# Kernel optimization log

Measured on AMD Instinct MI355X. Metric: run time of the kernel, lower is better.

## Reference

```python
import jax, jax.numpy as jnp
import numpy as np

K = 3
CHUNK = 1000  # query chunk size for KNN distance tiles
EPS = 1e-8
GRID = 256.0  # coordinate extent (coords / stride in the original)


def _knn3(queries, refs):
    """Brute-force KNN (K=3, squared L2) computed in chunks to bound memory.
    queries: [Q,3], refs: [M,3] -> (dist [Q,3], idx [Q,3] int32)."""
    ref_sq = jnp.sum(refs * refs, axis=-1)  # [M]

    def chunk_fn(q):  # q: [CHUNK,3]
        d = jnp.sum(q * q, -1)[:, None] - 2.0 * (q @ refs.T) + ref_sq[None, :]
        d = jnp.maximum(d, 0.0)  # guard tiny negatives from cancellation
        neg_d, idx = jax.lax.top_k(-d, K)
        return -neg_d, idx

    Q = queries.shape[0]
    qs = queries.reshape(Q // CHUNK, CHUNK, 3)
    dists, idxs = jax.lax.map(chunk_fn, qs)
    return dists.reshape(Q, K), idxs.reshape(Q, K)


def setup_inputs() -> dict:
    key = jax.random.key(0)
    k1, k2, k3, k4 = jax.random.split(key, 4)
    N1, N2, C = 20000, 20000, 8
    xyz1 = jax.random.uniform(k1, (N1, 3), dtype=jnp.float32) * GRID
    point1 = jax.random.normal(k2, (N1, C), dtype=jnp.float32)
    xyz2 = jax.random.uniform(k3, (N2, 3), dtype=jnp.float32) * GRID
    motion = jax.random.normal(k4, (N2, C, 3), dtype=jnp.float32)
    return {"xyz1": xyz1, "point1": point1, "xyz2": xyz2, "motion": motion}


def reference(xyz1, point1, xyz2, motion):
    # Motion-compensated inter prediction tail of inter_prediction.forward:
    # per-channel warp, KNN(K=3) into frame 1, inverse-distance interpolation.
    N2, C, _ = motion.shape
    # xyz2_ = xyz2.unsqueeze(2) + motion -> [N2*C, 3]
    xyz2_ = (xyz2[:, None, :] + motion).reshape(N2 * C, 3)
    dist, idx = _knn3(xyz2_, xyz1)                 # [N2*C,3]
    dist = dist + EPS
    dist = dist.reshape(N2, C, K)
    idx = idx.reshape(N2, C, K)
    weights = 1.0 / dist
    weights = weights / jnp.maximum(weights.sum(axis=2, keepdims=True), 3.0)
    # knn_point1[n,c,k] = point1[idx[n,c,k], c]  (per-channel gather)
    pt = point1.T                                   # [C, N1]
    knn_point1 = pt[jnp.arange(C)[None, :, None], idx]  # [N2,C,3]
    predicted_point2 = (weights * knn_point1).sum(axis=2)  # [N2,C]
    return predicted_point2
```

## Files before the change

kernel.cpp:

```cpp
#include <hip/hip_runtime.h>
#include <math.h>

#define KNN_EPS 1e-8f
#define GH 16.0f
#define GC 16
#define NCELLS (GC * GC * GC)
#define MARGIN 1.0f
#define CAP 384
#define CAPR 64
#define CAPQ 192


__device__ __forceinline__ int cell_coord(float v) {
    int c = (int)floorf(v * (1.0f / GH));
    return min(max(c, 0), GC - 1);
}

__global__ void fused_scatter_kernel(
    const float* __restrict__ xyz1, int n1,
    const float* __restrict__ xyz2,
    const float* __restrict__ motion, int n2, int C,
    int* __restrict__ counts, int* __restrict__ qcounts,
    float4* __restrict__ rbuck, float4* __restrict__ qbuck,
    float4* __restrict__ refspill, int* __restrict__ rsn,
    float4* __restrict__ qspill, int* __restrict__ qsn)
{
#pragma clang fp contract(off)
    int i = blockIdx.x * blockDim.x + threadIdx.x;
    if (i < n1) {
        float x = xyz1[3 * i + 0];
        float y = xyz1[3 * i + 1];
        float z = xyz1[3 * i + 2];
        int cid = (cell_coord(z) * GC + cell_coord(y)) * GC + cell_coord(x);
        int pos = atomicAdd(&counts[cid], 1);
        float4 v = make_float4(x, y, z, __int_as_float(i));
        if (pos < CAPR) rbuck[cid * CAPR + pos] = v;
        else { int sp = atomicAdd(rsn, 1); refspill[sp] = v; }
    }
    int nq = n2 * C;
    if (i < nq) {
        int n = i / C;
        float qx = xyz2[3 * n + 0] + motion[3 * i + 0];
        float qy = xyz2[3 * n + 1] + motion[3 * i + 1];
        float qz = xyz2[3 * n + 2] + motion[3 * i + 2];
        int cid = (cell_coord(qz) * GC + cell_coord(qy)) * GC + cell_coord(qx);
        int pos = atomicAdd(&qcounts[cid], 1);
        float4 v = make_float4(qx, qy, qz, __int_as_float(i));
        if (pos < CAPQ) qbuck[cid * CAPQ + pos] = v;
        else { int sp = atomicAdd(qsn, 1); qspill[sp] = v; }
    }
}

__device__ __forceinline__ void top3_insert_lex(float d, int j,
                                                float& bd0, float& bd1, float& bd2,
                                                int& bi0, int& bi1, int& bi2) {
    if (d < bd2 || (d == bd2 && j < bi2)) {
        if (d < bd1 || (d == bd1 && j < bi1)) {
            bd2 = bd1; bi2 = bi1;
            if (d < bd0 || (d == bd0 && j < bi0)) {
                bd1 = bd0; bi1 = bi0;
                bd0 = d;   bi0 = j;
            } else {
                bd1 = d;   bi1 = j;
            }
        } else {
            bd2 = d;       bi2 = j;
        }
    }
}

__device__ __forceinline__ void eval_candidate(
    float4 r, float qx, float qy, float qz, float qsq,
    float& bd0, float& bd1, float& bd2, int& bi0, int& bi1, int& bi2) {
    int ridx = __float_as_int(r.w);
    float rsq = r.x * r.x + r.y * r.y;
    rsq = rsq + r.z * r.z;
    float t = fmaf(qz, r.z, fmaf(qy, r.y, qx * r.x));
    float h = qsq + rsq;
    float d = fmaxf(fmaf(-2.0f, t, h), 0.0f);
    top3_insert_lex(d, ridx, bd0, bd1, bd2, bi0, bi1, bi2);
}

__device__ __forceinline__ float cert_radius(float qx, float qy, float qz,
                                             int icx, int icy, int icz, int rho) {
    float R = INFINITY;
    if (icx - rho > 0)      R = fminf(R, qx - (float)(icx - rho) * GH);
    if (icx + rho < GC - 1) R = fminf(R, (float)(icx + rho + 1) * GH - qx);
    if (icy - rho > 0)      R = fminf(R, qy - (float)(icy - rho) * GH);
    if (icy + rho < GC - 1) R = fminf(R, (float)(icy + rho + 1) * GH - qy);
    if (icz - rho > 0)      R = fminf(R, qz - (float)(icz - rho) * GH);
    if (icz + rho < GC - 1) R = fminf(R, (float)(icz + rho + 1) * GH - qz);
    return R;
}

__device__ __forceinline__ void epilogue_store(
    float bd0, float bd1, float bd2, int bi0, int bi1, int bi2,
    int qid, int C, const float* __restrict__ point1, float* __restrict__ out) {
#pragma clang fp contract(off)
    float dd0 = bd0 + KNN_EPS;
    float dd1 = bd1 + KNN_EPS;
    float dd2 = bd2 + KNN_EPS;
    float w0 = 1.0f / dd0;
    float w1 = 1.0f / dd1;
    float w2 = 1.0f / dd2;
    float s  = w0 + w1;
    s = s + w2;
    float m = fmaxf(s, 3.0f);
    w0 = w0 / m;
    w1 = w1 / m;
    w2 = w2 / m;
    const int c = qid - (qid / C) * C;
    float p0 = point1[bi0 * C + c];
    float p1 = point1[bi1 * C + c];
    float p2 = point1[bi2 * C + c];
    float acc = w0 * p0 + w1 * p1;
    acc = acc + w2 * p2;
    out[qid] = acc;
}

__device__ void ring_search(float qx, float qy, float qz, float qsq,
                            const float4* __restrict__ rbuck,
                            const int* __restrict__ counts, int rspn,
                            const float4* __restrict__ refspill,
                            float& bd0, float& bd1, float& bd2,
                            int& bi0, int& bi1, int& bi2) {
    const int icx = cell_coord(qx);
    const int icy = cell_coord(qy);
    const int icz = cell_coord(qz);
    for (int k = 0; k < rspn; ++k)
        eval_candidate(refspill[k], qx, qy, qz, qsq, bd0, bd1, bd2, bi0, bi1, bi2);
    for (int rho = 0; rho < GC; ++rho) {
        for (int dz = -rho; dz <= rho; ++dz) {
            int cz = icz + dz;
            if (cz < 0 || cz >= GC) continue;
            int adz = (dz < 0) ? -dz : dz;
            for (int dy = -rho; dy <= rho; ++dy) {
                int cy = icy + dy;
                if (cy < 0 || cy >= GC) continue;
                int ady = (dy < 0) ? -dy : dy;
                int step = (adz == rho || ady == rho || rho == 0) ? 1 : 2 * rho;
                for (int dx = -rho; dx <= rho; dx += step) {
                    int cx = icx + dx;
                    if (cx < 0 || cx >= GC) continue;
                    int cid = (cz * GC + cy) * GC + cx;
                    int e = min(counts[cid], CAPR);
                    for (int s = 0; s < e; ++s)
                        eval_candidate(rbuck[cid * CAPR + s], qx, qy, qz, qsq,
                                       bd0, bd1, bd2, bi0, bi1, bi2);
                }
            }
        }
        float Rr = cert_radius(qx, qy, qz, icx, icy, icz, rho);
        if (bd2 + MARGIN <= Rr * Rr) break;
    }
}

__global__ __launch_bounds__(128, 8) void knn_cell_kernel(
    const float4* __restrict__ rbuck,
    const int*   __restrict__ counts,
    const float4* __restrict__ refspill,
    const int*   __restrict__ rsn,
    const float4* __restrict__ qbuck,
    const int*   __restrict__ qcounts,
    const float* __restrict__ point1,
    float* __restrict__ out,
    int C)
{
#pragma clang fp contract(off)
    const int cell = blockIdx.x;
    const int qn = min(qcounts[cell], CAPQ);
    if (qn == 0) return;
    const int qbase = cell * CAPQ;

    const int tid = threadIdx.x;
    const int lane = tid & 63;
    const int wave = tid >> 6;

    const int icx = cell & (GC - 1);
    const int icy = (cell >> 4) & (GC - 1);
    const int icz = cell >> 8;

    __shared__ float4 cand[CAP];
    __shared__ int rcid[27], rlen[27], rofs[27], rst[27];
    __shared__ int total_s, ovf_s, rsn_s;
    __shared__ float pbd[64][3];
    __shared__ int   pbi[64][3];

    if (tid < 27) {
        int dz = tid / 9 - 1, dy = (tid / 3) % 3 - 1, dx = tid % 3 - 1;
        int cz = icz + dz, cy = icy + dy, cx = icx + dx;
        int ok = (cz >= 0 && cz < GC && cy >= 0 && cy < GC && cx >= 0 && cx < GC);
        int cid = ok ? (cz * GC + cy) * GC + cx : 0;
        rcid[tid] = cid;
        rlen[tid] = ok ? min(counts[cid], CAPR) : 0;
    }
    if (tid == 32) rsn_s = *rsn;
    __syncthreads();
    if (tid == 0) {
        int run = 0, ovf = 0;
        for (int r = 0; r < 27; ++r) {
            int len = rlen[r];
            int st = min(len, CAP - run);
            rofs[r] = run; rst[r] = st;
            run += st;
            if (st < len) ovf = 1;
        }
        total_s = run; ovf_s = ovf;
    }
    __syncthreads();

    const int total = total_s;
    const int ovf = ovf_s;
    const int rspn = rsn_s;

    for (int i = tid; i < total; i += 128) {
        int lo = 0, hi = 26;
        while (lo < hi) {
            int mid = (lo + hi + 1) >> 1;
            if (rofs[mid] <= i) lo = mid; else hi = mid - 1;
        }
        cand[i] = rbuck[rcid[lo] * CAPR + (i - rofs[lo])];
    }
    __syncthreads();

    const int half = total >> 1;
    const int k0 = wave ? half : 0;
    const int k1 = wave ? total : half;

    const int niter = (qn + 63) >> 6;
    for (int it = 0; it < niter; ++it) {
        const int qo = it * 64 + lane;
        const bool active = qo < qn;
        float4 Q = qbuck[qbase + (active ? qo : 0)];
        const float qx = Q.x, qy = Q.y, qz = Q.z;
        const int qid = __float_as_int(Q.w);
        float qsq = qx * qx + qy * qy;
        qsq = qsq + qz * qz;

        float bd0 = INFINITY, bd1 = INFINITY, bd2 = INFINITY;
        int   bi0 = 0,        bi1 = 0,        bi2 = 0;

        int k = k0;
        for (; k + 4 <= k1; k += 4) {
            float4 c0 = cand[k + 0];
            float4 c1 = cand[k + 1];
            float4 c2 = cand[k + 2];
            float4 c3 = cand[k + 3];
            eval_candidate(c0, qx, qy, qz, qsq, bd0, bd1, bd2, bi0, bi1, bi2);
            eval_candidate(c1, qx, qy, qz, qsq, bd0, bd1, bd2, bi0, bi1, bi2);
            eval_candidate(c2, qx, qy, qz, qsq, bd0, bd1, bd2, bi0, bi1, bi2);
            eval_candidate(c3, qx, qy, qz, qsq, bd0, bd1, bd2, bi0, bi1, bi2);
        }
        for (; k < k1; ++k)
            eval_candidate(cand[k], qx, qy, qz, qsq, bd0, bd1, bd2, bi0, bi1, bi2);

        if (wave == 1) {
            pbd[lane][0] = bd0; pbd[lane][1] = bd1; pbd[lane][2] = bd2;
            pbi[lane][0] = bi0; pbi[lane][1] = bi1; pbi[lane][2] = bi2;
        }
        __syncthreads();

        if (wave == 0) {
            for (int m = 0; m < 3; ++m) {
                float d = pbd[lane][m];
                if (d < INFINITY)
                    top3_insert_lex(d, pbi[lane][m], bd0, bd1, bd2, bi0, bi1, bi2);
            }
            for (int k2 = 0; k2 < rspn; ++k2)
                eval_candidate(refspill[k2], qx, qy, qz, qsq,
                               bd0, bd1, bd2, bi0, bi1, bi2);
            if (ovf) {
                for (int r = 0; r < 27; ++r)
                    for (int kk = rst[r]; kk < rlen[r]; ++kk)
                        eval_candidate(rbuck[rcid[r] * CAPR + kk], qx, qy, qz, qsq,
                                       bd0, bd1, bd2, bi0, bi1, bi2);
            }
            float R = cert_radius(qx, qy, qz, icx, icy, icz, 1);
            if (!(bd2 + MARGIN <= R * R)) {
                for (int rho = 2; rho < GC; ++rho) {
                    for (int dz = -rho; dz <= rho; ++dz) {
                        int cz = icz + dz;
                        if (cz < 0 || cz >= GC) continue;
                        int adz = (dz < 0) ? -dz : dz;
                        for (int dy = -rho; dy <= rho; ++dy) {
                            int cy = icy + dy;
                            if (cy < 0 || cy >= GC) continue;
                            int ady = (dy < 0) ? -dy : dy;
                            int step = (adz == rho || ady == rho) ? 1 : 2 * rho;
                            for (int dx = -rho; dx <= rho; dx += step) {
                                int cx = icx + dx;
                                if (cx < 0 || cx >= GC) continue;
                                int cid = (cz * GC + cy) * GC + cx;
                                int e = min(counts[cid], CAPR);
                                for (int s = 0; s < e; ++s)
                                    eval_candidate(rbuck[cid * CAPR + s],
                                                   qx, qy, qz, qsq,
                                                   bd0, bd1, bd2, bi0, bi1, bi2);
                            }
                        }
                    }
                    float Rr = cert_radius(qx, qy, qz, icx, icy, icz, rho);
                    if (bd2 + MARGIN <= Rr * Rr) break;
                }
            }

            if (active)
                epilogue_store(bd0, bd1, bd2, bi0, bi1, bi2, qid, C, point1, out);
        }
        if (it + 1 < niter) __syncthreads();
    }
}

__global__ __launch_bounds__(256) void qspill_kernel(
    const float4* __restrict__ qspill, const int* __restrict__ qsn,
    const float4* __restrict__ rbuck, const int* __restrict__ counts,
    const float4* __restrict__ refspill, const int* __restrict__ rsn,
    const float* __restrict__ point1, float* __restrict__ out, int C)
{
#pragma clang fp contract(off)
    const int nsp = *qsn;
    const int rspn = *rsn;
    for (int s = blockIdx.x * blockDim.x + threadIdx.x; s < nsp;
         s += gridDim.x * blockDim.x) {
        float4 Q = qspill[s];
        const float qx = Q.x, qy = Q.y, qz = Q.z;
        const int qid = __float_as_int(Q.w);
        float qsq = qx * qx + qy * qy;
        qsq = qsq + qz * qz;
        float bd0 = INFINITY, bd1 = INFINITY, bd2 = INFINITY;
        int   bi0 = 0,        bi1 = 0,        bi2 = 0;
        ring_search(qx, qy, qz, qsq, rbuck, counts, rspn, refspill,
                    bd0, bd1, bd2, bi0, bi1, bi2);
        epilogue_store(bd0, bd1, bd2, bi0, bi1, bi2, qid, C, point1, out);
    }
}

extern "C" void kernel_launch(void* const* d_in, const int* in_sizes, int n_in,
                              void* d_out, int out_size, void* d_ws, size_t ws_size,
                              hipStream_t stream) {
    const float* xyz1   = (const float*)d_in[0];
    const float* point1 = (const float*)d_in[1];
    const float* xyz2   = (const float*)d_in[2];
    const float* motion = (const float*)d_in[3];
    float* out = (float*)d_out;

    const int n1 = in_sizes[0] / 3;
    const int n2 = in_sizes[2] / 3;
    const int C  = in_sizes[1] / n1;
    const int nq = n2 * C;

    char* ws = (char*)d_ws;
    size_t off = 0;
    auto alloc = [&](size_t bytes) {
        char* p = ws + off;
        off = (off + bytes + 255) & ~(size_t)255;
        return p;
    };
    float4* rbuck    = (float4*)alloc((size_t)NCELLS * CAPR * 16);
    float4* qbuck    = (float4*)alloc((size_t)NCELLS * CAPQ * 16);
    float4* refspill = (float4*)alloc((size_t)n1 * 16);
    float4* qspill   = (float4*)alloc((size_t)nq * 16);
    int*    zero     = (int*)alloc((size_t)(2 * NCELLS + 2) * 4);
    int* counts  = zero;
    int* qcounts = zero + NCELLS;
    int* rsn     = zero + 2 * NCELLS;
    int* qsn     = zero + 2 * NCELLS + 1;

    const int nmax = (n1 > nq) ? n1 : nq;

    hipMemsetAsync(zero, 0, (size_t)(2 * NCELLS + 2) * 4, stream);
    fused_scatter_kernel<<<(nmax + 255) / 256, 256, 0, stream>>>(
        xyz1, n1, xyz2, motion, n2, C,
        counts, qcounts, rbuck, qbuck, refspill, rsn, qspill, qsn);
    knn_cell_kernel<<<NCELLS, 128, 0, stream>>>(
        rbuck, counts, refspill, rsn, qbuck, qcounts, point1, out, C);
    qspill_kernel<<<4, 256, 0, stream>>>(
        qspill, qsn, rbuck, counts, refspill, rsn, point1, out, C);
}
```

Before: 169.4 us.

## Fold query-spill pass into cell kernel, parallelize prefix, split top-3 accumulators

Handles spilled queries in four extra blocks of the cell KNN kernel instead of a separate launch, removing one kernel launch and its serialization. Replaces the single-thread prefix sum over the 27 neighbor cells with a per-thread computation. Splits the inner candidate loop into four independent top-3 accumulators that are merged afterwards, to break the dependency chain. The cost is higher register pressure under the 128x8 launch bounds and a merge step per query.

```diff
diff --git a/kernel.cpp b/kernel.cpp
--- a/kernel.cpp
+++ b/kernel.cpp
@@ -162,12 +162,33 @@
     const int*   __restrict__ rsn,
     const float4* __restrict__ qbuck,
     const int*   __restrict__ qcounts,
+    const float4* __restrict__ qspill,
+    const int*   __restrict__ qsn,
     const float* __restrict__ point1,
     float* __restrict__ out,
     int C)
 {
 #pragma clang fp contract(off)
     const int cell = blockIdx.x;
+
+    if (cell >= NCELLS) {
+        const int nsp = *qsn;
+        if (nsp == 0) return;
+        const int rspn = *rsn;
+        for (int s = (cell - NCELLS) * 128 + threadIdx.x; s < nsp; s += 4 * 128) {
+            float4 Q = qspill[s];
+            float qsq = Q.x * Q.x + Q.y * Q.y;
+            qsq = qsq + Q.z * Q.z;
+            float bd0 = INFINITY, bd1 = INFINITY, bd2 = INFINITY;
+            int   bi0 = 0,        bi1 = 0,        bi2 = 0;
+            ring_search(Q.x, Q.y, Q.z, qsq, rbuck, counts, rspn, refspill,
+                        bd0, bd1, bd2, bi0, bi1, bi2);
+            epilogue_store(bd0, bd1, bd2, bi0, bi1, bi2,
+                           __float_as_int(Q.w), C, point1, out);
+        }
+        return;
+    }
+
     const int qn = min(qcounts[cell], CAPQ);
     if (qn == 0) return;
     const int qbase = cell * CAPQ;
@@ -196,16 +217,14 @@
     }
     if (tid == 32) rsn_s = *rsn;
     __syncthreads();
-    if (tid == 0) {
-        int run = 0, ovf = 0;
-        for (int r = 0; r < 27; ++r) {
-            int len = rlen[r];
-            int st = min(len, CAP - run);
-            rofs[r] = run; rst[r] = st;
-            run += st;
-            if (st < len) ovf = 1;
-        }
-        total_s = run; ovf_s = ovf;
+    if (tid < 27) {
+        int run = 0;
+        for (int r = 0; r < tid; ++r) run += rlen[r];
+        int len = rlen[tid];
+        int st = max(0, min(len, CAP - run));
+        rofs[tid] = min(run, CAP);
+        rst[tid] = st;
+        if (tid == 26) { total_s = min(run + len, CAP); ovf_s = (run + len > CAP); }
     }
     __syncthreads();
 
@@ -237,8 +256,14 @@
         float qsq = qx * qx + qy * qy;
         qsq = qsq + qz * qz;
 
-        float bd0 = INFINITY, bd1 = INFINITY, bd2 = INFINITY;
-        int   bi0 = 0,        bi1 = 0,        bi2 = 0;
+        float Ad0 = INFINITY, Ad1 = INFINITY, Ad2 = INFINITY;
+        int   Ai0 = 0,        Ai1 = 0,        Ai2 = 0;
+        float Bd0 = INFINITY, Bd1 = INFINITY, Bd2 = INFINITY;
+        int   Bi0 = 0,        Bi1 = 0,        Bi2 = 0;
+        float Cd0 = INFINITY, Cd1 = INFINITY, Cd2 = INFINITY;
+        int   Ci0 = 0,        Ci1 = 0,        Ci2 = 0;
+        float Dd0 = INFINITY, Dd1 = INFINITY, Dd2 = INFINITY;
+        int   Di0 = 0,        Di1 = 0,        Di2 = 0;
 
         int k = k0;
         for (; k + 4 <= k1; k += 4) {
@@ -246,13 +271,25 @@
             float4 c1 = cand[k + 1];
             float4 c2 = cand[k + 2];
             float4 c3 = cand[k + 3];
-            eval_candidate(c0, qx, qy, qz, qsq, bd0, bd1, bd2, bi0, bi1, bi2);
-            eval_candidate(c1, qx, qy, qz, qsq, bd0, bd1, bd2, bi0, bi1, bi2);
-            eval_candidate(c2, qx, qy, qz, qsq, bd0, bd1, bd2, bi0, bi1, bi2);
-            eval_candidate(c3, qx, qy, qz, qsq, bd0, bd1, bd2, bi0, bi1, bi2);
+            eval_candidate(c0, qx, qy, qz, qsq, Ad0, Ad1, Ad2, Ai0, Ai1, Ai2);
+            eval_candidate(c1, qx, qy, qz, qsq, Bd0, Bd1, Bd2, Bi0, Bi1, Bi2);
+            eval_candidate(c2, qx, qy, qz, qsq, Cd0, Cd1, Cd2, Ci0, Ci1, Ci2);
+            eval_candidate(c3, qx, qy, qz, qsq, Dd0, Dd1, Dd2, Di0, Di1, Di2);
         }
         for (; k < k1; ++k)
-            eval_candidate(cand[k], qx, qy, qz, qsq, bd0, bd1, bd2, bi0, bi1, bi2);
+            eval_candidate(cand[k], qx, qy, qz, qsq, Ad0, Ad1, Ad2, Ai0, Ai1, Ai2);
+
+        float bd0 = Ad0, bd1 = Ad1, bd2 = Ad2;
+        int   bi0 = Ai0, bi1 = Ai1, bi2 = Ai2;
+        if (Bd0 < INFINITY) top3_insert_lex(Bd0, Bi0, bd0, bd1, bd2, bi0, bi1, bi2);
+        if (Bd1 < INFINITY) top3_insert_lex(Bd1, Bi1, bd0, bd1, bd2, bi0, bi1, bi2);
+        if (Bd2 < INFINITY) top3_insert_lex(Bd2, Bi2, bd0, bd1, bd2, bi0, bi1, bi2);
+        if (Cd0 < INFINITY) top3_insert_lex(Cd0, Ci0, bd0, bd1, bd2, bi0, bi1, bi2);
+        if (Cd1 < INFINITY) top3_insert_lex(Cd1, Ci1, bd0, bd1, bd2, bi0, bi1, bi2);
+        if (Cd2 < INFINITY) top3_insert_lex(Cd2, Ci2, bd0, bd1, bd2, bi0, bi1, bi2);
+        if (Dd0 < INFINITY) top3_insert_lex(Dd0, Di0, bd0, bd1, bd2, bi0, bi1, bi2);
+        if (Dd1 < INFINITY) top3_insert_lex(Dd1, Di1, bd0, bd1, bd2, bi0, bi1, bi2);
+        if (Dd2 < INFINITY) top3_insert_lex(Dd2, Di2, bd0, bd1, bd2, bi0, bi1, bi2);
 
         if (wave == 1) {
             pbd[lane][0] = bd0; pbd[lane][1] = bd1; pbd[lane][2] = bd2;
@@ -311,30 +348,6 @@
     }
 }
 
-__global__ __launch_bounds__(256) void qspill_kernel(
-    const float4* __restrict__ qspill, const int* __restrict__ qsn,
-    const float4* __restrict__ rbuck, const int* __restrict__ counts,
-    const float4* __restrict__ refspill, const int* __restrict__ rsn,
-    const float* __restrict__ point1, float* __restrict__ out, int C)
-{
-#pragma clang fp contract(off)
-    const int nsp = *qsn;
-    const int rspn = *rsn;
-    for (int s = blockIdx.x * blockDim.x + threadIdx.x; s < nsp;
-         s += gridDim.x * blockDim.x) {
-        float4 Q = qspill[s];
-        const float qx = Q.x, qy = Q.y, qz = Q.z;
-        const int qid = __float_as_int(Q.w);
-        float qsq = qx * qx + qy * qy;
-        qsq = qsq + qz * qz;
-        float bd0 = INFINITY, bd1 = INFINITY, bd2 = INFINITY;
-        int   bi0 = 0,        bi1 = 0,        bi2 = 0;
-        ring_search(qx, qy, qz, qsq, rbuck, counts, rspn, refspill,
-                    bd0, bd1, bd2, bi0, bi1, bi2);
-        epilogue_store(bd0, bd1, bd2, bi0, bi1, bi2, qid, C, point1, out);
-    }
-}
-
 extern "C" void kernel_launch(void* const* d_in, const int* in_sizes, int n_in,
                               void* d_out, int out_size, void* d_ws, size_t ws_size,
                               hipStream_t stream) {
@@ -372,8 +385,7 @@
     fused_scatter_kernel<<<(nmax + 255) / 256, 256, 0, stream>>>(
         xyz1, n1, xyz2, motion, n2, C,
         counts, qcounts, rbuck, qbuck, refspill, rsn, qspill, qsn);
-    knn_cell_kernel<<<NCELLS, 128, 0, stream>>>(
-        rbuck, counts, refspill, rsn, qbuck, qcounts, point1, out, C);
-    qspill_kernel<<<4, 256, 0, stream>>>(
-        qspill, qsn, rbuck, counts, refspill, rsn, point1, out, C);
-}
+    knn_cell_kernel<<<NCELLS + 4, 128, 0, stream>>>(
+        rbuck, counts, refspill, rsn, qbuck, qcounts, qspill, qsn,
+        point1, out, C);
+}
```

New measurement: 267.8 us. 1.58x slower.
